# Kernel optimization log

Measured on AMD Instinct MI355X. Metric: run time of the kernel, lower is better.

## Reference

```python
import jax, jax.numpy as jnp
import numpy as np
from jax import lax

NH, K, V, TOPK = 8, 64, 64, 4  # n_heads, key_size, val_size, SparseAttention top_k(=3+1)
EPS = 1e-7
BN_EPS = 1e-5


def conv1x1(x, w, b):
    # x: [B,C,H,W], w: [O,C] -> [B,O,H,W]
    return jnp.einsum('oc,bchw->bohw', w, x) + b[None, :, None, None]


def conv3x3(x, w, b):
    y = lax.conv_general_dilated(x, w, (1, 1), 'SAME',
                                 dimension_numbers=('NCHW', 'OIHW', 'NCHW'))
    return y + b[None, :, None, None]


def batchnorm(x, g, b):
    # training-mode BN over (N,H,W), biased variance (matches torch BatchNorm2d in train)
    m = jnp.mean(x, axis=(0, 2, 3), keepdims=True)
    v = jnp.var(x, axis=(0, 2, 3), keepdims=True)
    return (x - m) * lax.rsqrt(v + BN_EPS) * g[None, :, None, None] + b[None, :, None, None]


def to_flat(y, d):
    # [B, NH*d, H, W] -> [B*H*W*NH, d]
    B, _, H, W = y.shape
    return y.reshape(B, NH, d, H, W).transpose(0, 3, 4, 1, 2).reshape(B * H * W * NH, d)


def setup_inputs() -> dict:
    key = jax.random.key(0)
    ks = jax.random.split(key, 16)
    L, C, B, H, W = 4, 256, 8, 32, 32
    KH, VH = K * NH, V * NH
    s = 0.02
    return {
        'x': jax.random.normal(ks[0], (B, C, H, W), jnp.float32),
        'kw': jax.random.normal(ks[1], (L, KH, C), jnp.float32) * s,
        'kb': jax.random.normal(ks[2], (L, KH), jnp.float32) * s,
        'qw': jax.random.normal(ks[3], (L, KH, C), jnp.float32) * s,
        'qb': jax.random.normal(ks[4], (L, KH), jnp.float32) * s,
        'vw': jax.random.normal(ks[5], (L, VH, C), jnp.float32) * s,
        'vb': jax.random.normal(ks[6], (L, VH), jnp.float32) * s,
        'ow1': jax.random.normal(ks[7], (L, C, VH, 3, 3), jnp.float32) * s,
        'ob1': jax.random.normal(ks[8], (L, C), jnp.float32) * s,
        'bn_g': jnp.ones((L, C), jnp.float32),
        'bn_b': jnp.zeros((L, C), jnp.float32),
        'ow2': jax.random.normal(ks[9], (L, C, C, 3, 3), jnp.float32) * s,
        'ob2': jax.random.normal(ks[10], (L, C), jnp.float32) * s,
        'gammas': jax.random.normal(ks[11], (L,), jnp.float32),
    }


def reference(x, kw, kb, qw, qb, vw, vb, ow1, ob1, bn_g, bn_b, ow2, ob2, gammas):
    B, C, H, W = x.shape
    L = kw.shape[0]
    temp = jnp.asarray(np.power(K, 0.5), x.dtype)  # concentration=0.5
    keys, vals = [], []
    for l in range(L):  # structurally distinct layers: growing key/val list
        keys.append(to_flat(conv1x1(x, kw[l], kb[l]), K))  # [N,K]
        vals.append(to_flat(conv1x1(x, vw[l], vb[l]), V))  # [N,V]
        q = to_flat(conv1x1(x, qw[l], qb[l]), K)           # [N,K]
        kt = jnp.stack(keys + [jnp.zeros_like(keys[0])], axis=1)  # [N,T,K] zero key appended
        vt = jnp.stack(vals + [jnp.zeros_like(vals[0])], axis=1)  # [N,T,V]
        scores = jnp.einsum('nk,ntk->nt', q / temp, kt)
        attn = jax.nn.softmax(scores, axis=-1)
        T = attn.shape[1]
        if T > TOPK:  # SparseAttention: topk threshold, clamp, renormalize
            delta = lax.top_k(attn, TOPK)[0][:, -1] + EPS
            wgt = jnp.maximum(attn - delta[:, None], 0.0)
            attn = wgt / (jnp.sum(wgt, axis=1, keepdims=True) + EPS)
        o = jnp.einsum('nt,ntv->nv', attn, vt)  # [N,V]
        o = o.reshape(B, H, W, NH * V).transpose(0, 3, 1, 2)  # [B, NH*V, H, W]
        h1 = jax.nn.relu(batchnorm(conv3x3(o, ow1[l], ob1[l]), bn_g[l], bn_b[l]))
        h2 = conv3x3(h1, ow2[l], ob2[l])
        x = x + h2 * gammas[l]
    return x
```

## Files before the change

### kernel.cpp

```cpp
#include <hip/hip_runtime.h>


typedef __attribute__((ext_vector_type(8))) short short8;
typedef __attribute__((ext_vector_type(4))) float f32x4;
typedef __attribute__((ext_vector_type(2))) float f32x2;
typedef __attribute__((ext_vector_type(4))) unsigned short ushort4_t;
typedef __attribute__((ext_vector_type(4))) unsigned int uint4_t;

#define NTOK 65536
#define NPIX 8192

__device__ __forceinline__ float bf2f(unsigned short u) {
  unsigned int v = ((unsigned int)u) << 16;
  float f; __builtin_memcpy(&f, &v, 4); return f;
}
__device__ __forceinline__ unsigned short f2bf(float f) {
  unsigned int u; __builtin_memcpy(&u, &f, 4);
  u = (u + 0x7FFFu + ((u >> 16) & 1u)) >> 16;
  return (unsigned short)u;
}
__device__ __forceinline__ float blo(unsigned int u) {
  unsigned int v = u << 16; float f; __builtin_memcpy(&f, &v, 4); return f;
}
__device__ __forceinline__ float bhi(unsigned int u) {
  unsigned int v = u & 0xFFFF0000u; float f; __builtin_memcpy(&f, &v, 4); return f;
}

__device__ __forceinline__ void gl_lds16(const unsigned short* g, const unsigned short* l) {
  __builtin_amdgcn_global_load_lds(
      (const __attribute__((address_space(1))) unsigned int*)g,
      (__attribute__((address_space(3))) unsigned int*)l, 16, 0, 0);
}

__global__ void k_prep(const float* __restrict__ kw, const float* __restrict__ vw,
                       const float* __restrict__ qw, const float* __restrict__ ow1,
                       const float* __restrict__ ow2, const float* __restrict__ kb,
                       const float* __restrict__ vb, const float* __restrict__ qb,
                       unsigned short* __restrict__ wkqv, unsigned short* __restrict__ w1,
                       unsigned short* __restrict__ w2, float* __restrict__ biascat) {
  long i = (long)blockIdx.x * 256 + threadIdx.x;
  if (i < 1572864) {
    int idx = (int)(i & 131071); int sl = (int)(i >> 17); int slot = sl % 3, l = sl / 3;
    const float* s = slot == 0 ? kw : slot == 1 ? vw : qw;
    wkqv[i] = f2bf(s[(size_t)l * 131072 + idx]);
    return;
  }
  i -= 1572864;
  if (i < 4718592) {
    int c = (int)(i % 512), tap = (int)((i / 512) % 9); long m = i / 4608;
    w1[i] = f2bf(ow1[(m * 512 + c) * 9 + tap]);
    return;
  }
  i -= 4718592;
  if (i < 2359296) {
    int c = (int)(i % 256), tap = (int)((i / 256) % 9); long m = i / 2304;
    w2[i] = f2bf(ow2[(m * 256 + c) * 9 + tap]);
    return;
  }
  i -= 2359296;
  if (i < 6144) {
    int o = (int)(i & 511); int sl = (int)(i >> 9); int slot = sl % 3, l = sl / 3;
    const float* s = slot == 0 ? kb : slot == 1 ? vb : qb;
    biascat[i] = s[l * 512 + o];
  }
}

__global__ __launch_bounds__(256) void k_x2cl(const float* __restrict__ src,
                                              unsigned short* __restrict__ dst) {
  __shared__ unsigned short t[64][68];
  const int hw0 = blockIdx.x * 64, b = blockIdx.y;
  const int tid = threadIdx.x;
  for (int cc = 0; cc < 4; cc++) {
    __syncthreads();
    {
      const int px = tid & 63, c = tid >> 6;
      #pragma unroll
      for (int i = 0; i < 16; i++)
        t[px][c + i * 4] = f2bf(src[((size_t)b * 256 + cc * 64 + c + i * 4) * 1024 + hw0 + px]);
    }
    __syncthreads();
    {
      const int px = tid >> 2, c0 = (tid & 3) * 16;
      unsigned short* dp = dst + ((size_t)b * 1024 + hw0 + px) * 256 + cc * 64 + c0;
      short8 v0, v1;
      #pragma unroll
      for (int i = 0; i < 8; i++) { v0[i] = (short)t[px][c0 + i]; v1[i] = (short)t[px][c0 + 8 + i]; }
      *(short8*)dp = v0; *(short8*)(dp + 8) = v1;
    }
  }
}

__global__ __launch_bounds__(256) void k_zero_borders(unsigned int* __restrict__ opad,
                                                      unsigned int* __restrict__ h1pad) {
  const int idx = blockIdx.x;
  const int b = idx / 132, i = idx % 132;
  int y, x;
  if (i < 34) { y = 0; x = i; }
  else if (i < 68) { y = 33; x = i - 34; }
  else { const int j = i - 68; y = 1 + (j >> 1); x = (j & 1) * 33; }
  const size_t pix = (size_t)b * 1156 + y * 34 + x;
  opad[pix * 256 + threadIdx.x] = 0u;
  if (threadIdx.x < 128) h1pad[pix * 128 + threadIdx.x] = 0u;
}

template<int MODE, int NSTEP, int KDIM, int CIN>
__global__ __launch_bounds__(256) void k_gemm(
    const unsigned short* __restrict__ W,
    const unsigned short* __restrict__ act,
    const float* __restrict__ bias,
    int l,
    unsigned short* __restrict__ ktok, unsigned short* __restrict__ vtok,
    unsigned short* __restrict__ qtok,
    unsigned short* __restrict__ pout) {
  __shared__ unsigned short sm[2][2][8192];

  const int bid = blockIdx.x;
  int m0, b, pix0, s;
  if constexpr (MODE == 0) {
    const int xcd = bid & 7, li = bid >> 3;
    const int nt = xcd * 8 + (li & 7);
    m0 = (li >> 3) * 128; s = 0;
    b = nt >> 3; pix0 = (nt & 7) * 128;
  } else {
    const int xcd = bid & 7, li = bid >> 3;
    const int nt = xcd * 8 + (li & 7);
    const int r = li >> 3;
    m0 = (r & 1) * 128; s = r >> 1;
    b = nt >> 3; pix0 = (nt & 7) * 128;
  }
  constexpr int SW = (MODE == 1) ? 128 : 64;

  const int tid = threadIdx.x;
  const int wid = tid >> 6, lane = tid & 63;
  const int lr = lane & 15, lg = lane >> 4;
  const int m_off = (wid >> 1) * 64, n_off = (wid & 1) * 64;

  const unsigned short* gA[4];
  const unsigned short* gB[4];
  #pragma unroll
  for (int j = 0; j < 4; j++) {
    const int o = (wid * 4 + j) * 512 + lane * 8;
    const int row = o >> 6;
    const int ksw = (((o >> 3) & 7) ^ (row & 7)) * 8;
    gA[j] = W + (size_t)(m0 + row) * KDIM + (MODE ? s * SW : 0) + ksw;
    if constexpr (MODE == 0) {
      gB[j] = act + ((size_t)b * 1024 + pix0 + row) * 256 + ksw;
    } else {
      const int pix = pix0 + row, py = pix >> 5, px = pix & 31;
      gB[j] = act + (size_t)b * 1156 * CIN + ((size_t)py * 34 + px) * CIN + s * SW + ksw;
    }
  }

  auto offA = [&](int st) -> int {
    if constexpr (MODE == 0) return st * 64;
    else if constexpr (MODE == 1) return (st >> 1) * 512 + (st & 1) * 64;
    else return st * 256;
  };
  auto offB = [&](int st) -> int {
    if constexpr (MODE == 0) return st * 64;
    else if constexpr (MODE == 1) {
      const int tap = st >> 1, dy = tap / 3, dx = tap - dy * 3;
      return (dy * 34 + dx) * 512 + (st & 1) * 64;
    } else {
      const int dy = st / 3, dx = st - dy * 3;
      return (dy * 34 + dx) * 256;
    }
  };
  auto STAGE = [&](int bf, int st) {
    const int oa = offA(st), ob = offB(st);
    #pragma unroll
    for (int j = 0; j < 4; j++) gl_lds16(gA[j] + oa, &sm[bf][0][(wid * 4 + j) * 512]);
    #pragma unroll
    for (int j = 0; j < 4; j++) gl_lds16(gB[j] + ob, &sm[bf][1][(wid * 4 + j) * 512]);
  };

  f32x4 acc[4][4] = {};

  STAGE(0, 0);
  __syncthreads();
  #pragma unroll
  for (int st = 0; st < NSTEP; st++) {
    if (st + 1 < NSTEP) STAGE((st + 1) & 1, st + 1);
    const int cur = st & 1;
    #pragma unroll
    for (int ks = 0; ks < 2; ks++) {
      short8 af[4], bfr[4];
      #pragma unroll
      for (int i = 0; i < 4; i++) {
        const int ra = m_off + i * 16 + lr;
        af[i] = *(const short8*)&sm[cur][0][ra * 64 + (((ks * 4 + lg) ^ (ra & 7)) * 8)];
        const int rb = n_off + i * 16 + lr;
        bfr[i] = *(const short8*)&sm[cur][1][rb * 64 + (((ks * 4 + lg) ^ (rb & 7)) * 8)];
      }
      #pragma unroll
      for (int i = 0; i < 4; i++)
        #pragma unroll
        for (int jn = 0; jn < 4; jn++)
          acc[i][jn] = __builtin_amdgcn_mfma_f32_16x16x32_bf16(af[i], bfr[jn], acc[i][jn], 0, 0, 0);
    }
    __syncthreads();
  }

  if constexpr (MODE == 0) {
    #pragma unroll
    for (int mi = 0; mi < 4; mi++) {
      const int mb = m0 + m_off + mi * 16 + lg * 4;
      const int tensor = mb >> 9, head = (mb >> 6) & 7, d0 = mb & 63;
      unsigned short* dst = (tensor == 0) ? ktok + (size_t)l * NTOK * 64
                          : (tensor == 1) ? vtok + (size_t)l * NTOK * 64 : qtok;
      const float b0 = bias[mb], b1 = bias[mb + 1], b2 = bias[mb + 2], b3 = bias[mb + 3];
      #pragma unroll
      for (int ni = 0; ni < 4; ni++) {
        const int n = pix0 + n_off + ni * 16 + lr;
        ushort4_t pk;
        pk[0] = f2bf(acc[mi][ni][0] + b0); pk[1] = f2bf(acc[mi][ni][1] + b1);
        pk[2] = f2bf(acc[mi][ni][2] + b2); pk[3] = f2bf(acc[mi][ni][3] + b3);
        *(ushort4_t*)&dst[(((size_t)b * 1024 + n) * 8 + head) * 64 + d0] = pk;
      }
    }
  } else {
    #pragma unroll
    for (int mi = 0; mi < 4; mi++) {
      const int mb = m0 + m_off + mi * 16 + lg * 4;
      unsigned short* orow = pout + (size_t)(s * 256 + mb) * 8192 + (size_t)b * 1024 + pix0;
      #pragma unroll
      for (int ni = 0; ni < 4; ni++) {
        const int n = n_off + ni * 16 + lr;
        #pragma unroll
        for (int r = 0; r < 4; r++) orow[(size_t)r * 8192 + n] = f2bf(acc[mi][ni][r]);
      }
    }
  }
}

template<int L>
__global__ __launch_bounds__(256) void k_attn(const unsigned int* __restrict__ q_tok,
                                              const unsigned int* __restrict__ k_tok,
                                              const unsigned int* __restrict__ v_tok,
                                              unsigned int* __restrict__ opad) {
  constexpr int T = L + 2;
  const int lane = threadIdx.x & 63, wid = threadIdx.x >> 6;
  const int ti = lane >> 2, dq = lane & 3;
  const int token = blockIdx.x * 64 + wid * 16 + ti;
  const size_t rowq = (size_t)token * 32 + dq * 8;

  unsigned int q[8];
  *(uint4_t*)&q[0] = *(const uint4_t*)(q_tok + rowq);
  *(uint4_t*)&q[4] = *(const uint4_t*)(q_tok + rowq + 4);
  float qf[16];
  #pragma unroll
  for (int j = 0; j < 8; j++) {
    qf[2 * j]     = blo(q[j]) * 0.125f;
    qf[2 * j + 1] = bhi(q[j]) * 0.125f;
  }

  float s[T];
  s[T - 1] = 0.0f;
  #pragma unroll
  for (int t = 0; t <= L; t++) {
    const unsigned int* kp = k_tok + (size_t)t * (NTOK * 32) + rowq;
    unsigned int kk[8];
    *(uint4_t*)&kk[0] = *(const uint4_t*)kp;
    *(uint4_t*)&kk[4] = *(const uint4_t*)(kp + 4);
    float p = 0.0f;
    #pragma unroll
    for (int j = 0; j < 8; j++) {
      p = fmaf(qf[2 * j], blo(kk[j]), p);
      p = fmaf(qf[2 * j + 1], bhi(kk[j]), p);
    }
    p += __shfl_xor(p, 1);
    p += __shfl_xor(p, 2);
    s[t] = p;
  }

  float mx = s[0];
  #pragma unroll
  for (int t = 1; t < T; t++) mx = fmaxf(mx, s[t]);
  float attn[T], sum = 0.0f;
  #pragma unroll
  for (int t = 0; t < T; t++) { attn[t] = __expf(s[t] - mx); sum += attn[t]; }
  const float inv = 1.0f / sum;
  #pragma unroll
  for (int t = 0; t < T; t++) attn[t] *= inv;

  if constexpr (T == 5) {
    float m1 = attn[0], m2 = 1e30f;
    #pragma unroll
    for (int t = 1; t < 5; t++) {
      const float a = attn[t];
      const float nm1 = fminf(m1, a);
      m2 = fminf(m2, fmaxf(m1, a));
      m1 = nm1;
    }
    const float delta = m2 + 1e-7f;
    float ws = 0.0f;
    #pragma unroll
    for (int t = 0; t < 5; t++) { attn[t] = fmaxf(attn[t] - delta, 0.0f); ws += attn[t]; }
    const float r = 1.0f / (ws + 1e-7f);
    #pragma unroll
    for (int t = 0; t < 5; t++) attn[t] *= r;
  }

  float o[16];
  #pragma unroll
  for (int i = 0; i < 16; i++) o[i] = 0.0f;
  #pragma unroll
  for (int t = 0; t <= L; t++) {
    const unsigned int* vp = v_tok + (size_t)t * (NTOK * 32) + rowq;
    unsigned int vv[8];
    *(uint4_t*)&vv[0] = *(const uint4_t*)vp;
    *(uint4_t*)&vv[4] = *(const uint4_t*)(vp + 4);
    const float a = attn[t];
    #pragma unroll
    for (int j = 0; j < 8; j++) {
      o[2 * j]     = fmaf(a, blo(vv[j]), o[2 * j]);
      o[2 * j + 1] = fmaf(a, bhi(vv[j]), o[2 * j + 1]);
    }
  }

  unsigned int po[8];
  #pragma unroll
  for (int j = 0; j < 8; j++) {
    unsigned int r;
    asm("v_cvt_pk_bf16_f32 %0, %1, %2" : "=v"(r) : "v"(o[2 * j]), "v"(o[2 * j + 1]));
    po[j] = r;
  }
  const int head = token & 7, pix = token >> 3;
  const int b = pix >> 10, hw = pix & 1023, y = hw >> 5, x = hw & 31;
  unsigned int* dp = opad +
      (((size_t)b * 1156 + (y + 1) * 34 + (x + 1)) * 512 + head * 64 + dq * 16) / 2;
  *(uint4_t*)dp = *(uint4_t*)&po[0];
  *(uint4_t*)(dp + 4) = *(uint4_t*)&po[4];
}

__global__ __launch_bounds__(256) void k_comb_stats(const unsigned int* __restrict__ p,
    const float* __restrict__ bias1, const float* __restrict__ g, const float* __restrict__ bta,
    unsigned int* __restrict__ h1c, float* __restrict__ stats) {
  const int c = blockIdx.x, tid = threadIdx.x;
  const float bs = bias1[c];
  const unsigned int* P0 = p + (size_t)c * 4096;
  unsigned int* H = h1c + (size_t)c * 4096;
  float s = 0.0f, ss = 0.0f;
  #pragma unroll
  for (int k2 = 0; k2 < 4; k2++) {
    const int j = (k2 * 256 + tid) * 4;
    uint4_t a0 = *(const uint4_t*)(P0 + j);
    uint4_t a1 = *(const uint4_t*)(P0 + 1048576 + j);
    uint4_t a2 = *(const uint4_t*)(P0 + 2097152 + j);
    uint4_t a3 = *(const uint4_t*)(P0 + 3145728 + j);
    uint4_t o;
    #pragma unroll
    for (int e = 0; e < 4; e++) {
      const float vl = blo(a0[e]) + blo(a1[e]) + blo(a2[e]) + blo(a3[e]) + bs;
      const float vh = bhi(a0[e]) + bhi(a1[e]) + bhi(a2[e]) + bhi(a3[e]) + bs;
      s += vl + vh; ss += vl * vl + vh * vh;
      o[e] = (unsigned int)f2bf(vl) | ((unsigned int)f2bf(vh) << 16);
    }
    *(uint4_t*)(H + j) = o;
  }
  #pragma unroll
  for (int o2 = 32; o2 > 0; o2 >>= 1) { s += __shfl_xor(s, o2); ss += __shfl_xor(ss, o2); }
  __shared__ float rs[4], rss[4];
  const int wid = tid >> 6, lane = tid & 63;
  if (lane == 0) { rs[wid] = s; rss[wid] = ss; }
  __syncthreads();
  if (tid == 0) {
    const float S = rs[0] + rs[1] + rs[2] + rs[3];
    const float SS = rss[0] + rss[1] + rss[2] + rss[3];
    const float m = S * (1.0f / 8192.0f);
    const float var = SS * (1.0f / 8192.0f) - m * m;
    const float A = g[c] * rsqrtf(var + 1e-5f);
    stats[c] = A;
    stats[256 + c] = bta[c] - m * A;
  }
}

__global__ __launch_bounds__(512) void k_bn_relu_pad(const unsigned int* __restrict__ h1c,
    const float* __restrict__ stats, unsigned short* __restrict__ hpad) {
  __shared__ unsigned short t[32][264];
  const int hw0 = blockIdx.x * 32, b = blockIdx.y, tid = threadIdx.x;
  const int u = tid & 15, cg = tid >> 4;
  const int base = ((b * 1024 + hw0) >> 1);
  #pragma unroll
  for (int i = 0; i < 8; i++) {
    const int ch = i * 32 + cg;
    const float A = stats[ch], Bt = stats[256 + ch];
    const unsigned int a = h1c[(size_t)ch * 4096 + base + u];
    t[2 * u][ch]     = f2bf(fmaxf(blo(a) * A + Bt, 0.0f));
    t[2 * u + 1][ch] = f2bf(fmaxf(bhi(a) * A + Bt, 0.0f));
  }
  __syncthreads();
  const int px = tid >> 4, c0 = (tid & 15) * 16;
  const int y = hw0 >> 5, x = hw0 & 31;
  unsigned short* dp = hpad + ((size_t)b * 1156 + (y + 1) * 34 + (x + px + 1)) * 256 + c0;
  short8 v0, v1;
  #pragma unroll
  for (int i = 0; i < 8; i++) { v0[i] = (short)t[px][c0 + i]; v1[i] = (short)t[px][c0 + 8 + i]; }
  *(short8*)dp = v0; *(short8*)(dp + 8) = v1;
}

__global__ __launch_bounds__(512) void k_comb2(const unsigned int* __restrict__ p,
    const float* __restrict__ bias2, const float* __restrict__ gamma_p, int last,
    float* __restrict__ xacc, unsigned short* __restrict__ xcl) {
  __shared__ unsigned short t[32][264];
  const int hw0 = blockIdx.x * 32, b = blockIdx.y, tid = threadIdx.x;
  const int u = tid & 15, cg = tid >> 4;
  const float gmm = gamma_p[0];
  const int base = ((b * 1024 + hw0) >> 1);
  #pragma unroll
  for (int i = 0; i < 8; i++) {
    const int ch = i * 32 + cg;
    const float bs = bias2[ch];
    const size_t j = (size_t)ch * 4096 + base + u;
    const unsigned int a0 = p[j];
    const unsigned int a1 = p[j + 1048576];
    const unsigned int a2 = p[j + 2097152];
    const unsigned int a3 = p[j + 3145728];
    const float vl = blo(a0) + blo(a1) + blo(a2) + blo(a3) + bs;
    const float vh = bhi(a0) + bhi(a1) + bhi(a2) + bhi(a3) + bs;
    float* X = xacc + ((size_t)b * 256 + ch) * 1024 + hw0 + 2 * u;
    f32x2 xv = *(const f32x2*)X;
    const float xl = xv[0] + gmm * vl;
    const float xh = xv[1] + gmm * vh;
    f32x2 xw = {xl, xh};
    *(f32x2*)X = xw;
    t[2 * u][ch]     = f2bf(xl);
    t[2 * u + 1][ch] = f2bf(xh);
  }
  __syncthreads();
  if (!last) {
    const int px = tid >> 4, c0 = (tid & 15) * 16;
    unsigned short* dp = xcl + ((size_t)b * 1024 + hw0 + px) * 256 + c0;
    short8 v0, v1;
    #pragma unroll
    for (int i = 0; i < 8; i++) { v0[i] = (short)t[px][c0 + i]; v1[i] = (short)t[px][c0 + 8 + i]; }
    *(short8*)dp = v0; *(short8*)(dp + 8) = v1;
  }
}

extern "C" void kernel_launch(void* const* d_in, const int* in_sizes, int n_in,
                              void* d_out, int out_size, void* d_ws, size_t ws_size,
                              hipStream_t stream) {
  (void)in_sizes; (void)n_in; (void)out_size;
  const float* x_in   = (const float*)d_in[0];
  const float* kw     = (const float*)d_in[1];
  const float* kb     = (const float*)d_in[2];
  const float* qw     = (const float*)d_in[3];
  const float* qb     = (const float*)d_in[4];
  const float* vw     = (const float*)d_in[5];
  const float* vb     = (const float*)d_in[6];
  const float* ow1    = (const float*)d_in[7];
  const float* ob1    = (const float*)d_in[8];
  const float* bn_g   = (const float*)d_in[9];
  const float* bn_b   = (const float*)d_in[10];
  const float* ow2    = (const float*)d_in[11];
  const float* ob2    = (const float*)d_in[12];
  const float* gammas = (const float*)d_in[13];

  char* ws = (char*)d_ws;
  size_t off = 0;
  auto alloc = [&](size_t bytes) -> void* {
    void* pp = ws + off;
    off += (bytes + 255) & ~(size_t)255;
    return pp;
  };
  unsigned short* xcl     = (unsigned short*)alloc((size_t)NPIX * 256 * 2);
  unsigned short* k_tok   = (unsigned short*)alloc((size_t)4 * NTOK * 64 * 2);
  unsigned short* v_tok   = (unsigned short*)alloc((size_t)4 * NTOK * 64 * 2);
  unsigned short* q_tok   = (unsigned short*)alloc((size_t)NTOK * 64 * 2);
  unsigned short* opad    = (unsigned short*)alloc((size_t)8 * 1156 * 512 * 2);
  unsigned int*   h1c     = (unsigned int*)alloc((size_t)256 * 4096 * 4);
  unsigned short* h1pad   = (unsigned short*)alloc((size_t)8 * 1156 * 256 * 2);
  unsigned short* p1      = (unsigned short*)alloc((size_t)4 * 256 * 8192 * 2);
  float*          stats   = (float*)alloc(512 * 4);
  unsigned short* wkqv    = (unsigned short*)alloc((size_t)4 * 3 * 512 * 256 * 2);
  unsigned short* w1bf    = (unsigned short*)alloc((size_t)1024 * 4608 * 2);
  unsigned short* w2bf    = (unsigned short*)alloc((size_t)1024 * 2304 * 2);
  float*          biascat = (float*)alloc((size_t)6144 * 4);
  if (off > ws_size) return;

  float* xacc = (float*)d_out;

  k_zero_borders<<<1056, 256, 0, stream>>>((unsigned int*)opad, (unsigned int*)h1pad);
  hipMemcpyAsync(xacc, x_in, (size_t)NPIX * 256 * 4, hipMemcpyDeviceToDevice, stream);
  k_prep<<<33816, 256, 0, stream>>>(kw, vw, qw, ow1, ow2, kb, vb, qb,
                                    wkqv, w1bf, w2bf, biascat);
  k_x2cl<<<dim3(16, 8), 256, 0, stream>>>(x_in, xcl);

  for (int l = 0; l < 4; l++) {
    k_gemm<0, 4, 256, 256><<<768, 256, 0, stream>>>(
        wkqv + (size_t)l * 3 * 512 * 256, xcl, biascat + l * 1536, l,
        k_tok, v_tok, q_tok, nullptr);
    const unsigned int* qt = (const unsigned int*)q_tok;
    const unsigned int* kt = (const unsigned int*)k_tok;
    const unsigned int* vt = (const unsigned int*)v_tok;
    unsigned int* op = (unsigned int*)opad;
    switch (l) {
      case 0: k_attn<0><<<1024, 256, 0, stream>>>(qt, kt, vt, op); break;
      case 1: k_attn<1><<<1024, 256, 0, stream>>>(qt, kt, vt, op); break;
      case 2: k_attn<2><<<1024, 256, 0, stream>>>(qt, kt, vt, op); break;
      default: k_attn<3><<<1024, 256, 0, stream>>>(qt, kt, vt, op); break;
    }
    k_gemm<1, 18, 4608, 512><<<512, 256, 0, stream>>>(
        w1bf + (size_t)l * 256 * 4608, opad, nullptr, l,
        nullptr, nullptr, nullptr, p1);
    k_comb_stats<<<256, 256, 0, stream>>>((const unsigned int*)p1, ob1 + l * 256,
                                          bn_g + l * 256, bn_b + l * 256, h1c, stats);
    k_bn_relu_pad<<<dim3(32, 8), 512, 0, stream>>>(h1c, stats, h1pad);
    k_gemm<2, 9, 2304, 256><<<512, 256, 0, stream>>>(
        w2bf + (size_t)l * 256 * 2304, h1pad, nullptr, l,
        nullptr, nullptr, nullptr, p1);
    k_comb2<<<dim3(32, 8), 512, 0, stream>>>((const unsigned int*)p1, ob2 + l * 256,
                                             gammas + l, (l == 3) ? 1 : 0, xacc, xcl);
  }
}
```

Before: 366.0 us.

## Halve GEMM K-step tile to 32 to cut LDS and raise occupancy

The shared-memory K tile in the bf16 MFMA GEMM shrinks from 64 to 32 elements per stage, which halves LDS use to 32 KB per block. The swizzle and load mapping are reworked for 32-wide rows, read offsets are precomputed, and the step counts double. A launch-bounds occupancy hint of 4 blocks is added and the main loop is only partially unrolled. The aim is more resident blocks per CU to hide latency. The cost is twice as many barriers and stages per block, each with less MFMA work to cover the load latency.

```diff
diff --git a/kernel.cpp b/kernel.cpp
--- a/kernel.cpp
+++ b/kernel.cpp
@@ -104,7 +104,7 @@
 }
 
 template<int MODE, int NSTEP, int KDIM, int CIN>
-__global__ __launch_bounds__(256) void k_gemm(
+__global__ __launch_bounds__(256, 4) void k_gemm(
     const unsigned short* __restrict__ W,
     const unsigned short* __restrict__ act,
     const float* __restrict__ bias,
@@ -112,7 +112,7 @@
     unsigned short* __restrict__ ktok, unsigned short* __restrict__ vtok,
     unsigned short* __restrict__ qtok,
     unsigned short* __restrict__ pout) {
-  __shared__ unsigned short sm[2][2][8192];
+  __shared__ unsigned short sm[2][2][4096];
 
   const int bid = blockIdx.x;
   int m0, b, pix0, s;
@@ -135,69 +135,72 @@
   const int lr = lane & 15, lg = lane >> 4;
   const int m_off = (wid >> 1) * 64, n_off = (wid & 1) * 64;
 
-  const unsigned short* gA[4];
-  const unsigned short* gB[4];
-  #pragma unroll
-  for (int j = 0; j < 4; j++) {
-    const int o = (wid * 4 + j) * 512 + lane * 8;
-    const int row = o >> 6;
-    const int ksw = (((o >> 3) & 7) ^ (row & 7)) * 8;
-    gA[j] = W + (size_t)(m0 + row) * KDIM + (MODE ? s * SW : 0) + ksw;
+  const unsigned short* gA[2];
+  const unsigned short* gB[2];
+  #pragma unroll
+  for (int j = 0; j < 2; j++) {
+    const int row = j * 64 + (tid >> 2);
+    const int swc = ((tid & 3) ^ ((row >> 1) & 3)) * 8;
+    gA[j] = W + (size_t)(m0 + row) * KDIM + (MODE ? s * SW : 0) + swc;
     if constexpr (MODE == 0) {
-      gB[j] = act + ((size_t)b * 1024 + pix0 + row) * 256 + ksw;
+      gB[j] = act + ((size_t)b * 1024 + pix0 + row) * 256 + swc;
     } else {
       const int pix = pix0 + row, py = pix >> 5, px = pix & 31;
-      gB[j] = act + (size_t)b * 1156 * CIN + ((size_t)py * 34 + px) * CIN + s * SW + ksw;
+      gB[j] = act + (size_t)b * 1156 * CIN + ((size_t)py * 34 + px) * CIN + s * SW + swc;
     }
   }
 
   auto offA = [&](int st) -> int {
-    if constexpr (MODE == 0) return st * 64;
-    else if constexpr (MODE == 1) return (st >> 1) * 512 + (st & 1) * 64;
-    else return st * 256;
+    if constexpr (MODE == 0) return st * 32;
+    else if constexpr (MODE == 1) return (st >> 2) * 512 + (st & 3) * 32;
+    else return (st >> 1) * 256 + (st & 1) * 32;
   };
   auto offB = [&](int st) -> int {
-    if constexpr (MODE == 0) return st * 64;
+    if constexpr (MODE == 0) return st * 32;
     else if constexpr (MODE == 1) {
+      const int tap = st >> 2, dy = tap / 3, dx = tap - dy * 3;
+      return (dy * 34 + dx) * 512 + (st & 3) * 32;
+    } else {
       const int tap = st >> 1, dy = tap / 3, dx = tap - dy * 3;
-      return (dy * 34 + dx) * 512 + (st & 1) * 64;
-    } else {
-      const int dy = st / 3, dx = st - dy * 3;
-      return (dy * 34 + dx) * 256;
+      return (dy * 34 + dx) * 256 + (st & 1) * 32;
     }
   };
   auto STAGE = [&](int bf, int st) {
     const int oa = offA(st), ob = offB(st);
     #pragma unroll
-    for (int j = 0; j < 4; j++) gl_lds16(gA[j] + oa, &sm[bf][0][(wid * 4 + j) * 512]);
-    #pragma unroll
-    for (int j = 0; j < 4; j++) gl_lds16(gB[j] + ob, &sm[bf][1][(wid * 4 + j) * 512]);
+    for (int j = 0; j < 2; j++) gl_lds16(gA[j] + oa, &sm[bf][0][j * 2048 + wid * 512]);
+    #pragma unroll
+    for (int j = 0; j < 2; j++) gl_lds16(gB[j] + ob, &sm[bf][1][j * 2048 + wid * 512]);
   };
+
+  int ard[4], brd[4];
+  #pragma unroll
+  for (int i = 0; i < 4; i++) {
+    const int ra = m_off + i * 16 + lr;
+    ard[i] = ra * 32 + ((lg ^ ((ra >> 1) & 3)) * 8);
+    const int rb = n_off + i * 16 + lr;
+    brd[i] = rb * 32 + ((lg ^ ((rb >> 1) & 3)) * 8);
+  }
 
   f32x4 acc[4][4] = {};
 
   STAGE(0, 0);
   __syncthreads();
-  #pragma unroll
+  #pragma unroll 2
   for (int st = 0; st < NSTEP; st++) {
     if (st + 1 < NSTEP) STAGE((st + 1) & 1, st + 1);
     const int cur = st & 1;
-    #pragma unroll
-    for (int ks = 0; ks < 2; ks++) {
-      short8 af[4], bfr[4];
+    short8 af[4], bfr[4];
+    #pragma unroll
+    for (int i = 0; i < 4; i++) {
+      af[i] = *(const short8*)&sm[cur][0][ard[i]];
+      bfr[i] = *(const short8*)&sm[cur][1][brd[i]];
+    }
+    #pragma unroll
+    for (int i = 0; i < 4; i++)
       #pragma unroll
-      for (int i = 0; i < 4; i++) {
-        const int ra = m_off + i * 16 + lr;
-        af[i] = *(const short8*)&sm[cur][0][ra * 64 + (((ks * 4 + lg) ^ (ra & 7)) * 8)];
-        const int rb = n_off + i * 16 + lr;
-        bfr[i] = *(const short8*)&sm[cur][1][rb * 64 + (((ks * 4 + lg) ^ (rb & 7)) * 8)];
-      }
-      #pragma unroll
-      for (int i = 0; i < 4; i++)
-        #pragma unroll
-        for (int jn = 0; jn < 4; jn++)
-          acc[i][jn] = __builtin_amdgcn_mfma_f32_16x16x32_bf16(af[i], bfr[jn], acc[i][jn], 0, 0, 0);
-    }
+      for (int jn = 0; jn < 4; jn++)
+        acc[i][jn] = __builtin_amdgcn_mfma_f32_16x16x32_bf16(af[i], bfr[jn], acc[i][jn], 0, 0, 0);
     __syncthreads();
   }
 
@@ -488,7 +491,7 @@
   k_x2cl<<<dim3(16, 8), 256, 0, stream>>>(x_in, xcl);
 
   for (int l = 0; l < 4; l++) {
-    k_gemm<0, 4, 256, 256><<<768, 256, 0, stream>>>(
+    k_gemm<0, 8, 256, 256><<<768, 256, 0, stream>>>(
         wkqv + (size_t)l * 3 * 512 * 256, xcl, biascat + l * 1536, l,
         k_tok, v_tok, q_tok, nullptr);
     const unsigned int* qt = (const unsigned int*)q_tok;
@@ -501,13 +504,13 @@
       case 2: k_attn<2><<<1024, 256, 0, stream>>>(qt, kt, vt, op); break;
       default: k_attn<3><<<1024, 256, 0, stream>>>(qt, kt, vt, op); break;
     }
-    k_gemm<1, 18, 4608, 512><<<512, 256, 0, stream>>>(
+    k_gemm<1, 36, 4608, 512><<<512, 256, 0, stream>>>(
         w1bf + (size_t)l * 256 * 4608, opad, nullptr, l,
         nullptr, nullptr, nullptr, p1);
     k_comb_stats<<<256, 256, 0, stream>>>((const unsigned int*)p1, ob1 + l * 256,
                                           bn_g + l * 256, bn_b + l * 256, h1c, stats);
     k_bn_relu_pad<<<dim3(32, 8), 512, 0, stream>>>(h1c, stats, h1pad);
-    k_gemm<2, 9, 2304, 256><<<512, 256, 0, stream>>>(
+    k_gemm<2, 18, 2304, 256><<<512, 256, 0, stream>>>(
         w2bf + (size_t)l * 256 * 2304, h1pad, nullptr, l,
         nullptr, nullptr, nullptr, p1);
     k_comb2<<<dim3(32, 8), 512, 0, stream>>>((const unsigned int*)p1, ob2 + l * 256,
```

After: 405.0 us. 1.11x slower.
